# Performance work log

Hardware: AMD Instinct MI355X
Metric: run time of the kernel (lower is better)

The kernel has to match this reference:

```python
import jax, jax.numpy as jnp
import numpy as np

TEMPERATURE = 8.0  # sqrt(head_dim=64)
NEG_INF = -1e9


def setup_inputs() -> dict:
    key = jax.random.key(0)
    kq, kk, kv, km = jax.random.split(key, 4)
    B, H, S, D = 2, 16, 2048, 64
    q = jax.random.normal(kq, (B, H, S, D), dtype=jnp.float32)
    k = jax.random.normal(kk, (B, H, S, D), dtype=jnp.float32)
    v = jax.random.normal(kv, (B, H, S, D), dtype=jnp.float32)
    mask = jax.random.randint(km, (B, 1, 1, S), 0, 2, dtype=jnp.int32)
    return {"q": q, "k": k, "v": v, "mask": mask}


def reference(q, k, v, mask):
    # attn = (q / T) @ k^T  -> [B,H,S,S]
    scores = jnp.einsum("bhqd,bhkd->bhqk", q / TEMPERATURE, k)
    scores = jnp.where(mask == 0, NEG_INF, scores)
    attn = jax.nn.softmax(scores, axis=-1)  # dropout is identity in eval mode
    output = jnp.einsum("bhqk,bhkd->bhqd", attn, v)
    return (output, attn)
```

## Files before the change

### kernel.cpp

```cpp
#include <hip/hip_runtime.h>
#include <stdint.h>

constexpr int S   = 2048;
constexpr int D   = 64;
constexpr int BH  = 32;
constexpr int QT  = 64;
constexpr int KT  = 64;
constexpr int LDP = 72;

using short8  = __attribute__((ext_vector_type(8))) short;
using float4v = __attribute__((ext_vector_type(4))) float;

static __device__ __forceinline__ unsigned short f2bf(float f) {
    union { float f; unsigned u; } x; x.f = f;
    unsigned u = x.u;
    u += 0x7fffu + ((u >> 16) & 1u);
    return (unsigned short)(u >> 16);
}

__global__ __launch_bounds__(256) void cvt_kernel(const float* __restrict__ src,
                                                  unsigned short* __restrict__ dst) {
#pragma unroll
    for (int i = 0; i < 4; ++i) {
        const size_t f4 = (size_t)blockIdx.x * 1024 + i * 256 + threadIdx.x;
        float4v val = ((const float4v*)src)[f4];
        ushort4 pk;
        pk.x = f2bf(val.x);
        pk.y = f2bf(val.y);
        pk.z = f2bf(val.z);
        pk.w = f2bf(val.w);
        ((ushort4*)dst)[f4] = pk;
    }
}

__global__ __launch_bounds__(256) void vt_kernel(const float* __restrict__ v,
                                                 unsigned short* __restrict__ vt) {
    __shared__ __align__(16) unsigned short sT[64][LDP];
    const int blk = blockIdx.x;
    const int bh  = blk >> 5;
    const int k0  = (blk & 31) << 6;
    const int t   = threadIdx.x;
    const float* vp = v + ((size_t)bh * S + k0) * D;
#pragma unroll
    for (int i = 0; i < 4; ++i) {
        const int f4 = t + 256 * i;
        float4v val = ((const float4v*)vp)[f4];
        const int e = f4 * 4;
        const int r = e >> 6;
        const int c = e & 63;
        sT[c + 0][r] = f2bf(val.x);
        sT[c + 1][r] = f2bf(val.y);
        sT[c + 2][r] = f2bf(val.z);
        sT[c + 3][r] = f2bf(val.w);
    }
    __syncthreads();
#pragma unroll
    for (int i = 0; i < 2; ++i) {
        const int f    = t + 256 * i;
        const int drow = f >> 3;
        const int kc   = (f & 7) * 8;
        short8 val = *(const short8*)&sT[drow][kc];
        *(short8*)(vt + ((size_t)bh * D + drow) * S + k0 + kc) = val;
    }
}

__global__ __launch_bounds__(256, 4) void attn_kernel(const float* __restrict__ q,
                                                      const unsigned short* __restrict__ kb,
                                                      const int* __restrict__ mask,
                                                      const unsigned short* __restrict__ vt,
                                                      float* __restrict__ out) {
    __shared__ __align__(16) unsigned short sQ[QT][LDP];
    __shared__ __align__(16) unsigned short sK[KT][LDP];
    __shared__ __align__(16) unsigned short sVt[D][LDP];
    __shared__ __align__(16) unsigned short sP[4][16][LDP];

    const int tid  = threadIdx.x;
    const int wave = tid >> 6;
    const int lane = tid & 63;
    const int quad = lane >> 4;
    const int n16  = lane & 15;

    const int bx0 = blockIdx.x;
    const int bx  = (bx0 & 7) * 128 + (bx0 >> 3);
    const int bh  = bx >> 5;
    const int qt  = bx & 31;
    const int q0  = qt * QT;
    const int b   = bh >> 4;

    const float* qp = q + ((size_t)bh * S + q0) * D;
    const unsigned short* kp  = kb + (size_t)bh * S * D;
    const unsigned short* vtp = vt + (size_t)bh * D * S;
    const int* mp = mask + b * S;

    {
        const float4v* src = (const float4v*)qp;
#pragma unroll
        for (int i = 0; i < 4; ++i) {
            const int f4 = tid + 256 * i;
            float4v val = src[f4];
            const int e = f4 * 4;
            const int row = e >> 6, col = e & 63;
            ushort4 pk;
            pk.x = f2bf(val.x * 0.125f);
            pk.y = f2bf(val.y * 0.125f);
            pk.z = f2bf(val.z * 0.125f);
            pk.w = f2bf(val.w * 0.125f);
            *(ushort4*)&sQ[row][col] = pk;
        }
    }
    __syncthreads();

    const short8 aq0 = *(const short8*)&sQ[wave * 16 + n16][quad * 8];
    const short8 aq1 = *(const short8*)&sQ[wave * 16 + n16][32 + quad * 8];

    float4v accO[4];
    const float4v zero4 = {0.f, 0.f, 0.f, 0.f};
#pragma unroll
    for (int nv = 0; nv < 4; ++nv) accO[nv] = zero4;
    float lsum[4] = {0.f, 0.f, 0.f, 0.f};

    for (int kt = 0; kt < S / KT; ++kt) {
        const int k0 = kt * KT;
        __syncthreads();
        {
            const unsigned short* ks = kp + (size_t)k0 * D;
#pragma unroll
            for (int i = 0; i < 2; ++i) {
                const int f = tid + 256 * i;
                short8 val = *(const short8*)(ks + f * 8);
                *(short8*)&sK[f >> 3][(f & 7) * 8] = val;
            }
#pragma unroll
            for (int i = 0; i < 2; ++i) {
                const int f    = tid + 256 * i;
                const int drow = f >> 3;
                const int kc8  = (f & 7) * 8;
                short8 val = *(const short8*)(vtp + (size_t)drow * S + k0 + kc8);
                *(short8*)&sVt[drow][kc8] = val;
            }
        }
        __syncthreads();

        float4v cf[4];
#pragma unroll
        for (int nc = 0; nc < 4; ++nc) cf[nc] = zero4;
        __builtin_amdgcn_s_setprio(1);
#pragma unroll
        for (int c = 0; c < 2; ++c) {
            const short8 a = (c == 0) ? aq0 : aq1;
#pragma unroll
            for (int nc = 0; nc < 4; ++nc) {
                const short8 bfr = *(const short8*)&sK[nc * 16 + n16][c * 32 + quad * 8];
                cf[nc] = __builtin_amdgcn_mfma_f32_16x16x32_bf16(a, bfr, cf[nc], 0, 0, 0);
            }
        }
        __builtin_amdgcn_s_setprio(0);

        float pv_[4][4];
#pragma unroll
        for (int nc = 0; nc < 4; ++nc) {
            const int mvi = mp[k0 + nc * 16 + n16];
#pragma unroll
            for (int r = 0; r < 4; ++r)
                pv_[nc][r] = mvi ? __expf(cf[nc][r]) : 0.f;
        }
#pragma unroll
        for (int r = 0; r < 4; ++r) {
            float s = pv_[0][r] + pv_[1][r] + pv_[2][r] + pv_[3][r];
            s += __shfl_xor(s, 1, 64);
            s += __shfl_xor(s, 2, 64);
            s += __shfl_xor(s, 4, 64);
            s += __shfl_xor(s, 8, 64);
            lsum[r] += s;
        }
#pragma unroll
        for (int nc = 0; nc < 4; ++nc)
#pragma unroll
            for (int r = 0; r < 4; ++r)
                sP[wave][quad * 4 + r][nc * 16 + n16] = f2bf(pv_[nc][r]);

        __builtin_amdgcn_s_setprio(1);
#pragma unroll
        for (int kc = 0; kc < 2; ++kc) {
            const short8 ap = *(const short8*)&sP[wave][n16][kc * 32 + quad * 8];
#pragma unroll
            for (int nv = 0; nv < 4; ++nv) {
                const short8 bv = *(const short8*)&sVt[nv * 16 + n16][kc * 32 + quad * 8];
                accO[nv] = __builtin_amdgcn_mfma_f32_16x16x32_bf16(ap, bv, accO[nv], 0, 0, 0);
            }
        }
        __builtin_amdgcn_s_setprio(0);
    }

    float linv[4];
#pragma unroll
    for (int r = 0; r < 4; ++r) linv[r] = 1.0f / lsum[r];

    {
        const size_t obase = ((size_t)bh * S + q0 + wave * 16) * D;
#pragma unroll
        for (int nv = 0; nv < 4; ++nv)
#pragma unroll
            for (int r = 0; r < 4; ++r)
                out[obase + (size_t)(quad * 4 + r) * D + nv * 16 + n16] = accO[nv][r] * linv[r];
    }

    float* attn = out + (size_t)BH * S * D;
    const size_t abase = (size_t)bh * S * S + (size_t)(q0 + wave * 16) * S;
    const int t4 = n16 & 3;
    const int g4 = n16 >> 2;
    for (int kt = 0; kt < S / KT; ++kt) {
        const int k0 = kt * KT;
        __syncthreads();
        {
            const unsigned short* ks = kp + (size_t)k0 * D;
#pragma unroll
            for (int i = 0; i < 2; ++i) {
                const int f = tid + 256 * i;
                short8 val = *(const short8*)(ks + f * 8);
                *(short8*)&sK[f >> 3][(f & 7) * 8] = val;
            }
        }
        __syncthreads();

        float4v cf[4];
#pragma unroll
        for (int nc = 0; nc < 4; ++nc) cf[nc] = zero4;
        __builtin_amdgcn_s_setprio(1);
#pragma unroll
        for (int c = 0; c < 2; ++c) {
            const short8 a = (c == 0) ? aq0 : aq1;
#pragma unroll
            for (int nc = 0; nc < 4; ++nc) {
                const short8 bfr = *(const short8*)&sK[nc * 16 + n16][c * 32 + quad * 8];
                cf[nc] = __builtin_amdgcn_mfma_f32_16x16x32_bf16(a, bfr, cf[nc], 0, 0, 0);
            }
        }
        __builtin_amdgcn_s_setprio(0);

#pragma unroll
        for (int nc = 0; nc < 4; ++nc) {
            const int mvi = mp[k0 + nc * 16 + n16];
            float m0 = mvi ? __expf(cf[nc][0]) * linv[0] : 0.f;
            float m1 = mvi ? __expf(cf[nc][1]) * linv[1] : 0.f;
            float m2 = mvi ? __expf(cf[nc][2]) * linv[2] : 0.f;
            float m3 = mvi ? __expf(cf[nc][3]) * linv[3] : 0.f;
            float s1_0 = __shfl_xor(m1, 1, 64);
            float s1_1 = __shfl_xor(m0, 1, 64);
            float s1_2 = __shfl_xor(m3, 1, 64);
            float s1_3 = __shfl_xor(m2, 1, 64);
            float n0 = (t4 & 1) ? s1_0 : m0;
            float n1 = (t4 & 1) ? m1 : s1_1;
            float n2 = (t4 & 1) ? s1_2 : m2;
            float n3 = (t4 & 1) ? m3 : s1_3;
            float s2_0 = __shfl_xor(n2, 2, 64);
            float s2_1 = __shfl_xor(n3, 2, 64);
            float s2_2 = __shfl_xor(n0, 2, 64);
            float s2_3 = __shfl_xor(n1, 2, 64);
            float4v w;
            w[0] = (t4 & 2) ? s2_0 : n0;
            w[1] = (t4 & 2) ? s2_1 : n1;
            w[2] = (t4 & 2) ? n2 : s2_2;
            w[3] = (t4 & 2) ? n3 : s2_3;
            *(float4v*)&attn[abase + (size_t)(quad * 4 + t4) * S + k0 + nc * 16 + g4 * 4] = w;
        }
    }
}

extern "C" void kernel_launch(void* const* d_in, const int* in_sizes, int n_in,
                              void* d_out, int out_size, void* d_ws, size_t ws_size,
                              hipStream_t stream) {
    const float* q    = (const float*)d_in[0];
    const float* k    = (const float*)d_in[1];
    const float* v    = (const float*)d_in[2];
    const int*   mask = (const int*)d_in[3];
    unsigned short* kbf = (unsigned short*)d_ws;
    unsigned short* vt  = kbf + (size_t)BH * S * D;
    float* out = (float*)d_out;

    cvt_kernel<<<dim3(1024), dim3(256), 0, stream>>>(k, kbf);
    vt_kernel<<<dim3(BH * (S / 64)), dim3(256), 0, stream>>>(v, vt);
    attn_kernel<<<dim3(BH * (S / QT)), dim3(256), 0, stream>>>(q, kbf, mask, vt, out);
}
```

Before: 713.7 us.

## Drop LDS staging; load K/V fragments directly and transpose S via register shuffles

```diff
diff --git a/kernel.cpp b/kernel.cpp
--- a/kernel.cpp
+++ b/kernel.cpp
@@ -16,6 +16,12 @@
     unsigned u = x.u;
     u += 0x7fffu + ((u >> 16) & 1u);
     return (unsigned short)(u >> 16);
+}
+
+static __device__ __forceinline__ unsigned cvt_pk_bf16(float lo, float hi) {
+    unsigned r;
+    asm("v_cvt_pk_bf16_f32 %0, %1, %2" : "=v"(r) : "v"(lo), "v"(hi));
+    return r;
 }
 
 __global__ __launch_bounds__(256) void cvt_kernel(const float* __restrict__ src,
@@ -69,11 +75,6 @@
                                                       const int* __restrict__ mask,
                                                       const unsigned short* __restrict__ vt,
                                                       float* __restrict__ out) {
-    __shared__ __align__(16) unsigned short sQ[QT][LDP];
-    __shared__ __align__(16) unsigned short sK[KT][LDP];
-    __shared__ __align__(16) unsigned short sVt[D][LDP];
-    __shared__ __align__(16) unsigned short sP[4][16][LDP];
-
     const int tid  = threadIdx.x;
     const int wave = tid >> 6;
     const int lane = tid & 63;
@@ -92,54 +93,31 @@
     const unsigned short* vtp = vt + (size_t)bh * D * S;
     const int* mp = mask + b * S;
 
+    short8 aq0, aq1;
     {
-        const float4v* src = (const float4v*)qp;
-#pragma unroll
-        for (int i = 0; i < 4; ++i) {
-            const int f4 = tid + 256 * i;
-            float4v val = src[f4];
-            const int e = f4 * 4;
-            const int row = e >> 6, col = e & 63;
-            ushort4 pk;
-            pk.x = f2bf(val.x * 0.125f);
-            pk.y = f2bf(val.y * 0.125f);
-            pk.z = f2bf(val.z * 0.125f);
-            pk.w = f2bf(val.w * 0.125f);
-            *(ushort4*)&sQ[row][col] = pk;
-        }
-    }
-    __syncthreads();
-
-    const short8 aq0 = *(const short8*)&sQ[wave * 16 + n16][quad * 8];
-    const short8 aq1 = *(const short8*)&sQ[wave * 16 + n16][32 + quad * 8];
+        const float4v* qrow = (const float4v*)(qp + (size_t)(wave * 16 + n16) * D);
+        float4v a = qrow[quad * 2], bq = qrow[quad * 2 + 1];
+        float4v c = qrow[8 + quad * 2], d = qrow[8 + quad * 2 + 1];
+        union { short8 s8; unsigned short u[8]; } t0, t1;
+        t0.u[0] = f2bf(a.x * 0.125f);  t0.u[1] = f2bf(a.y * 0.125f);
+        t0.u[2] = f2bf(a.z * 0.125f);  t0.u[3] = f2bf(a.w * 0.125f);
+        t0.u[4] = f2bf(bq.x * 0.125f); t0.u[5] = f2bf(bq.y * 0.125f);
+        t0.u[6] = f2bf(bq.z * 0.125f); t0.u[7] = f2bf(bq.w * 0.125f);
+        t1.u[0] = f2bf(c.x * 0.125f);  t1.u[1] = f2bf(c.y * 0.125f);
+        t1.u[2] = f2bf(c.z * 0.125f);  t1.u[3] = f2bf(c.w * 0.125f);
+        t1.u[4] = f2bf(d.x * 0.125f);  t1.u[5] = f2bf(d.y * 0.125f);
+        t1.u[6] = f2bf(d.z * 0.125f);  t1.u[7] = f2bf(d.w * 0.125f);
+        aq0 = t0.s8; aq1 = t1.s8;
+    }
 
     float4v accO[4];
     const float4v zero4 = {0.f, 0.f, 0.f, 0.f};
 #pragma unroll
     for (int nv = 0; nv < 4; ++nv) accO[nv] = zero4;
-    float lsum[4] = {0.f, 0.f, 0.f, 0.f};
+    float lsum = 0.f;
 
     for (int kt = 0; kt < S / KT; ++kt) {
         const int k0 = kt * KT;
-        __syncthreads();
-        {
-            const unsigned short* ks = kp + (size_t)k0 * D;
-#pragma unroll
-            for (int i = 0; i < 2; ++i) {
-                const int f = tid + 256 * i;
-                short8 val = *(const short8*)(ks + f * 8);
-                *(short8*)&sK[f >> 3][(f & 7) * 8] = val;
-            }
-#pragma unroll
-            for (int i = 0; i < 2; ++i) {
-                const int f    = tid + 256 * i;
-                const int drow = f >> 3;
-                const int kc8  = (f & 7) * 8;
-                short8 val = *(const short8*)(vtp + (size_t)drow * S + k0 + kc8);
-                *(short8*)&sVt[drow][kc8] = val;
-            }
-        }
-        __syncthreads();
 
         float4v cf[4];
 #pragma unroll
@@ -147,54 +125,82 @@
         __builtin_amdgcn_s_setprio(1);
 #pragma unroll
         for (int c = 0; c < 2; ++c) {
-            const short8 a = (c == 0) ? aq0 : aq1;
+            const short8 aq = (c == 0) ? aq0 : aq1;
 #pragma unroll
             for (int nc = 0; nc < 4; ++nc) {
-                const short8 bfr = *(const short8*)&sK[nc * 16 + n16][c * 32 + quad * 8];
-                cf[nc] = __builtin_amdgcn_mfma_f32_16x16x32_bf16(a, bfr, cf[nc], 0, 0, 0);
+                const short8 kf = *(const short8*)(kp + (size_t)(k0 + nc * 16 + n16) * D + c * 32 + quad * 8);
+                cf[nc] = __builtin_amdgcn_mfma_f32_16x16x32_bf16(kf, aq, cf[nc], 0, 0, 0);
             }
         }
         __builtin_amdgcn_s_setprio(0);
 
-        float pv_[4][4];
+        float p[4][4];
 #pragma unroll
         for (int nc = 0; nc < 4; ++nc) {
-            const int mvi = mp[k0 + nc * 16 + n16];
-#pragma unroll
-            for (int r = 0; r < 4; ++r)
-                pv_[nc][r] = mvi ? __expf(cf[nc][r]) : 0.f;
-        }
-#pragma unroll
-        for (int r = 0; r < 4; ++r) {
-            float s = pv_[0][r] + pv_[1][r] + pv_[2][r] + pv_[3][r];
-            s += __shfl_xor(s, 1, 64);
-            s += __shfl_xor(s, 2, 64);
-            s += __shfl_xor(s, 4, 64);
-            s += __shfl_xor(s, 8, 64);
-            lsum[r] += s;
-        }
-#pragma unroll
-        for (int nc = 0; nc < 4; ++nc)
-#pragma unroll
-            for (int r = 0; r < 4; ++r)
-                sP[wave][quad * 4 + r][nc * 16 + n16] = f2bf(pv_[nc][r]);
+            const int4 m4 = *(const int4*)(mp + k0 + nc * 16 + quad * 4);
+            p[nc][0] = m4.x ? __expf(cf[nc][0]) : 0.f;
+            p[nc][1] = m4.y ? __expf(cf[nc][1]) : 0.f;
+            p[nc][2] = m4.z ? __expf(cf[nc][2]) : 0.f;
+            p[nc][3] = m4.w ? __expf(cf[nc][3]) : 0.f;
+        }
+        {
+            float s = 0.f;
+#pragma unroll
+            for (int nc = 0; nc < 4; ++nc)
+#pragma unroll
+                for (int r = 0; r < 4; ++r) s += p[nc][r];
+            s += __shfl_xor(s, 16, 64);
+            s += __shfl_xor(s, 32, 64);
+            lsum += s;
+        }
+
+        unsigned w[8];
+#pragma unroll
+        for (int nc = 0; nc < 4; ++nc) {
+            w[nc * 2 + 0] = cvt_pk_bf16(p[nc][0], p[nc][1]);
+            w[nc * 2 + 1] = cvt_pk_bf16(p[nc][2], p[nc][3]);
+        }
+        unsigned X[4] = { w[0], w[1], w[4], w[5] };
+        unsigned Y[4] = { w[2], w[3], w[6], w[7] };
+        unsigned r1[4], r2[4];
+#pragma unroll
+        for (int d = 0; d < 4; ++d) {
+            const unsigned send1 = (quad & 2) ? X[d] : Y[d];
+            r1[d] = (unsigned)__shfl_xor((int)send1, 32, 64);
+        }
+#pragma unroll
+        for (int d = 0; d < 4; ++d) {
+            const unsigned send2 = (quad == 1) ? X[d] : (quad == 2) ? Y[d] : r1[d];
+            r2[d] = (unsigned)__shfl_xor((int)send2, 16, 64);
+        }
+        union { short8 s8; unsigned u[4]; } ap0, ap1;
+        ap0.u[0] = (quad == 0) ? w[0] : (quad == 2) ? r1[0] : r2[0];
+        ap0.u[1] = (quad == 0) ? w[1] : (quad == 2) ? r1[1] : r2[1];
+        ap0.u[2] = (quad == 3) ? w[2] : (quad == 1) ? r1[0] : r2[0];
+        ap0.u[3] = (quad == 3) ? w[3] : (quad == 1) ? r1[1] : r2[1];
+        ap1.u[0] = (quad == 0) ? w[4] : (quad == 2) ? r1[2] : r2[2];
+        ap1.u[1] = (quad == 0) ? w[5] : (quad == 2) ? r1[3] : r2[3];
+        ap1.u[2] = (quad == 3) ? w[6] : (quad == 1) ? r1[2] : r2[2];
+        ap1.u[3] = (quad == 3) ? w[7] : (quad == 1) ? r1[3] : r2[3];
 
         __builtin_amdgcn_s_setprio(1);
 #pragma unroll
         for (int kc = 0; kc < 2; ++kc) {
-            const short8 ap = *(const short8*)&sP[wave][n16][kc * 32 + quad * 8];
+            const short8 ap = (kc == 0) ? ap0.s8 : ap1.s8;
 #pragma unroll
             for (int nv = 0; nv < 4; ++nv) {
-                const short8 bv = *(const short8*)&sVt[nv * 16 + n16][kc * 32 + quad * 8];
+                const short8 bv = *(const short8*)(vtp + (size_t)(nv * 16 + n16) * S + k0 + kc * 32 + quad * 8);
                 accO[nv] = __builtin_amdgcn_mfma_f32_16x16x32_bf16(ap, bv, accO[nv], 0, 0, 0);
             }
         }
         __builtin_amdgcn_s_setprio(0);
     }
 
-    float linv[4];
-#pragma unroll
-    for (int r = 0; r < 4; ++r) linv[r] = 1.0f / lsum[r];
+    const float linv_sw = 1.0f / lsum;
+    float linv_c[4];
+#pragma unroll
+    for (int r = 0; r < 4; ++r)
+        linv_c[r] = __shfl(linv_sw, quad * 4 + r, 64);
 
     {
         const size_t obase = ((size_t)bh * S + q0 + wave * 16) * D;
@@ -202,67 +208,36 @@
         for (int nv = 0; nv < 4; ++nv)
 #pragma unroll
             for (int r = 0; r < 4; ++r)
-                out[obase + (size_t)(quad * 4 + r) * D + nv * 16 + n16] = accO[nv][r] * linv[r];
+                out[obase + (size_t)(quad * 4 + r) * D + nv * 16 + n16] = accO[nv][r] * linv_c[r];
     }
 
     float* attn = out + (size_t)BH * S * D;
-    const size_t abase = (size_t)bh * S * S + (size_t)(q0 + wave * 16) * S;
-    const int t4 = n16 & 3;
-    const int g4 = n16 >> 2;
+    const size_t arow = (size_t)bh * S * S + (size_t)(q0 + wave * 16 + n16) * S;
     for (int kt = 0; kt < S / KT; ++kt) {
         const int k0 = kt * KT;
-        __syncthreads();
-        {
-            const unsigned short* ks = kp + (size_t)k0 * D;
-#pragma unroll
-            for (int i = 0; i < 2; ++i) {
-                const int f = tid + 256 * i;
-                short8 val = *(const short8*)(ks + f * 8);
-                *(short8*)&sK[f >> 3][(f & 7) * 8] = val;
-            }
-        }
-        __syncthreads();
-
         float4v cf[4];
 #pragma unroll
         for (int nc = 0; nc < 4; ++nc) cf[nc] = zero4;
         __builtin_amdgcn_s_setprio(1);
 #pragma unroll
         for (int c = 0; c < 2; ++c) {
-            const short8 a = (c == 0) ? aq0 : aq1;
+            const short8 aq = (c == 0) ? aq0 : aq1;
 #pragma unroll
             for (int nc = 0; nc < 4; ++nc) {
-                const short8 bfr = *(const short8*)&sK[nc * 16 + n16][c * 32 + quad * 8];
-                cf[nc] = __builtin_amdgcn_mfma_f32_16x16x32_bf16(a, bfr, cf[nc], 0, 0, 0);
+                const short8 kf = *(const short8*)(kp + (size_t)(k0 + nc * 16 + n16) * D + c * 32 + quad * 8);
+                cf[nc] = __builtin_amdgcn_mfma_f32_16x16x32_bf16(kf, aq, cf[nc], 0, 0, 0);
             }
         }
         __builtin_amdgcn_s_setprio(0);
-
 #pragma unroll
         for (int nc = 0; nc < 4; ++nc) {
-            const int mvi = mp[k0 + nc * 16 + n16];
-            float m0 = mvi ? __expf(cf[nc][0]) * linv[0] : 0.f;
-            float m1 = mvi ? __expf(cf[nc][1]) * linv[1] : 0.f;
-            float m2 = mvi ? __expf(cf[nc][2]) * linv[2] : 0.f;
-            float m3 = mvi ? __expf(cf[nc][3]) * linv[3] : 0.f;
-            float s1_0 = __shfl_xor(m1, 1, 64);
-            float s1_1 = __shfl_xor(m0, 1, 64);
-            float s1_2 = __shfl_xor(m3, 1, 64);
-            float s1_3 = __shfl_xor(m2, 1, 64);
-            float n0 = (t4 & 1) ? s1_0 : m0;
-            float n1 = (t4 & 1) ? m1 : s1_1;
-            float n2 = (t4 & 1) ? s1_2 : m2;
-            float n3 = (t4 & 1) ? m3 : s1_3;
-            float s2_0 = __shfl_xor(n2, 2, 64);
-            float s2_1 = __shfl_xor(n3, 2, 64);
-            float s2_2 = __shfl_xor(n0, 2, 64);
-            float s2_3 = __shfl_xor(n1, 2, 64);
-            float4v w;
-            w[0] = (t4 & 2) ? s2_0 : n0;
-            w[1] = (t4 & 2) ? s2_1 : n1;
-            w[2] = (t4 & 2) ? n2 : s2_2;
-            w[3] = (t4 & 2) ? n3 : s2_3;
-            *(float4v*)&attn[abase + (size_t)(quad * 4 + t4) * S + k0 + nc * 16 + g4 * 4] = w;
+            const int4 m4 = *(const int4*)(mp + k0 + nc * 16 + quad * 4);
+            float4v wv;
+            wv[0] = m4.x ? __expf(cf[nc][0]) * linv_sw : 0.f;
+            wv[1] = m4.y ? __expf(cf[nc][1]) * linv_sw : 0.f;
+            wv[2] = m4.z ? __expf(cf[nc][2]) * linv_sw : 0.f;
+            wv[3] = m4.w ? __expf(cf[nc][3]) * linv_sw : 0.f;
+            *(float4v*)&attn[arow + k0 + nc * 16 + quad * 4] = wv;
         }
     }
 }
```

New measurement: 906.7 us. +27.0%, slower.
